# Performance work log

Measured on AMD Instinct MI355X. Metric: run time of the kernel, lower is better.

Reference implementation:

```python
import jax, jax.numpy as jnp
import numpy as np

N_USERS = 50000
N_ITEMS = 50000
N = N_USERS + N_ITEMS
C = 5        # n_criterion
D = 64       # emb_dim
A = 32       # att_dim
L = 2        # n_layers
E = 1600000  # edges per criterion
ALPHA = 0.3  # keras LeakyReLU default

def leaky(x):
    return jnp.where(x >= 0, x, ALPHA * x)

def setup_inputs() -> dict:
    key = jax.random.key(0)
    ks = jax.random.split(key, 11)
    return {
        "rows": jax.random.randint(ks[0], (C, E), 0, N),
        "cols": jax.random.randint(ks[1], (C, E), 0, N),
        "vals": jax.random.uniform(ks[2], (C, E), dtype=jnp.float32) * 0.01,
        "user_emb": 0.01 * jax.random.normal(ks[3], (N_USERS, C, D), dtype=jnp.float32),
        "item_emb": 0.01 * jax.random.normal(ks[4], (N_ITEMS, C, D), dtype=jnp.float32),
        "cri_emb": 0.01 * jax.random.normal(ks[5], (C, D), dtype=jnp.float32),
        "w_gcn": 0.01 * jax.random.normal(ks[6], (D, D), dtype=jnp.float32),
        "W_gc": 0.01 * jax.random.normal(ks[7], (L, D, D), dtype=jnp.float32),
        "W_rel": 0.01 * jax.random.normal(ks[8], (L, D, D), dtype=jnp.float32),
        "W1": 0.01 * jax.random.normal(ks[9], (C, D, A), dtype=jnp.float32),
        "W2": 0.01 * jax.random.normal(ks[10], (C, A), dtype=jnp.float32),
    }

def _spmm(r, c, v, x):
    # one criterion: sparse [N,N] (COO r,c,v) @ dense x [N,D]
    return jax.ops.segment_sum(v[:, None] * x[c], r, num_segments=N)

def reference(rows, cols, vals, user_emb, item_emb, cri_emb, w_gcn, W_gc, W_rel, W1, W2):
    pre = jnp.concatenate([user_emb, item_emb], axis=0)  # [N, C, D]
    acc = pre
    cri_cur = cri_emb                                    # [C, D]
    cri_hist = [cri_cur]
    for k in range(L):
        x = jnp.swapaxes(pre, 0, 1)                      # [C, N, D]
        emb = jax.vmap(_spmm)(rows, cols, vals, x)       # [C, N, D]
        emb = emb @ w_gcn                                # per-criterion dense transform
        emb = leaky((emb * cri_cur[:, None, :]) @ W_gc[k])
        emb_st = jnp.swapaxes(emb, 0, 1)                 # [N, C, D]
        # attention over criteria, one (W1,W2) pair per output criterion i
        s = jnp.einsum('ncd,ida->nica', emb_st, W1)      # [N, C_out, C_in, A]
        s = jnp.einsum('nica,ia->nic', jnp.tanh(s), W2)  # [N, C_out, C_in]
        attn = jax.nn.softmax(s, axis=2)
        pre = leaky(jnp.einsum('nic,ncd->nid', attn, emb_st))  # [N, C, D]
        acc = acc + pre                                  # dropout inactive (training=False)
        cri_cur = leaky(cri_cur @ W_rel[k])
        cri_hist.append(cri_cur)
    acc = acc / (L + 1)
    users = acc[:N_USERS]
    items = jnp.concatenate([acc[N_USERS:], jnp.zeros((1, C, D), acc.dtype)], axis=0)
    cri_mean = jnp.mean(jnp.stack(cri_hist, axis=0), axis=0)  # [C, D]
    return users, items, cri_mean
```

## Files before the change

kernel.cpp:

```cpp
#include <hip/hip_runtime.h>
#include <hip/hip_bf16.h>

#define NU      50000
#define NT      100000
#define NPADR   100032
#define NC      5
#define DD      64
#define AA      32
#define EE      1600000
#define CE      (NC*EE)
#define ROWF    (NC*DD)
#define NBL     1563
#define OUT_ELEMS 32000000

#define NBIN    782
#define BROWS   128
#define SBLK    250
#define EPB     6400
#define EPT     25
#define KTOT    (NC*NBIN*SBLK)
#define S1B     1910
#define LCAP    2560

#define TMP_OFF   0
#define XB_OFF    64020480
#define EBIN_OFF  128040960
#define HW_OFF    192040960
#define BSUM_OFF  195950960
#define BST_OFF   195958600
#define CRI1_OFF  195974244
#define WC_OFF    195975536
#define W1B_OFF   196057456

using short8 = __attribute__((ext_vector_type(8))) short;
using f32x4  = __attribute__((ext_vector_type(4))) float;

__device__ __forceinline__ f32x4 mfma16(short8 a, short8 b, f32x4 c){
  return __builtin_amdgcn_mfma_f32_16x16x32_bf16(a, b, c, 0, 0, 0);
}
__device__ __forceinline__ float lk(float x){ return x >= 0.f ? x : 0.3f*x; }
__device__ __forceinline__ float fast_tanh(float x){
  float e = __expf(2.0f*x);
  return (e - 1.0f) * __builtin_amdgcn_rcpf(e + 1.0f);
}
__device__ __forceinline__ float bf2f(unsigned u){ return __uint_as_float(u << 16); }
__device__ __forceinline__ unsigned short f2bf_rn(float f){
  unsigned b = __float_as_uint(f);
  return (unsigned short)((b + 0x7FFFu + ((b >> 16) & 1u)) >> 16);
}

__global__ __launch_bounds__(256) void dmcr_cvt(const float* __restrict__ ue,
                                                const float* __restrict__ ie,
                                                unsigned short* __restrict__ xb){
  size_t idx = ((size_t)blockIdx.x*256 + threadIdx.x) * 4;
  const float* src = (idx < (size_t)NU*ROWF) ? (ue + idx) : (ie + (idx - (size_t)NU*ROWF));
  float4 f = *(const float4*)src;
  ushort4 h;
  h.x = f2bf_rn(f.x); h.y = f2bf_rn(f.y); h.z = f2bf_rn(f.z); h.w = f2bf_rn(f.w);
  *(ushort4*)(xb + idx) = h;
}

__global__ __launch_bounds__(256) void dmcr_hist(const int* __restrict__ rows,
                                                 unsigned* __restrict__ hw){
  __shared__ unsigned hist[NBIN];
  const int c = blockIdx.y, blk = blockIdx.x, t = threadIdx.x;
  for (int i=t; i<NBIN; i+=256) hist[i] = 0u;
  __syncthreads();
  const size_t g0 = (size_t)c*EE + (size_t)blk*EPB;
  #pragma unroll
  for (int k=0; k<EPT; k++){
    int r = rows[g0 + t + k*256];
    atomicAdd(&hist[r>>7], 1u);
  }
  __syncthreads();
  unsigned* dst = hw + (size_t)(c*SBLK + blk)*NBIN;
  for (int i=t; i<NBIN; i+=256) dst[i] = hist[i];
}

__global__ __launch_bounds__(512) void dmcr_scan1(unsigned* __restrict__ hw,
                                                  unsigned* __restrict__ bsum){
  __shared__ unsigned sh[512];
  const int t = threadIdx.x; const int s = blockIdx.x*512 + t;
  unsigned v = 0u; size_t st = 0; const bool ok = (s < KTOT);
  if (ok){
    int c = s / (NBIN*SBLK); int rem = s - c*(NBIN*SBLK);
    int bin = rem / SBLK;    int blk = rem - bin*SBLK;
    st = (size_t)(c*SBLK + blk)*NBIN + bin;
    v = hw[st];
  }
  sh[t] = v; __syncthreads();
  for (int off=1; off<512; off<<=1){
    unsigned x = (t>=off) ? sh[t-off] : 0u; __syncthreads();
    sh[t] += x; __syncthreads();
  }
  if (ok) hw[st] = sh[t] - v;
  if (t == 511) bsum[blockIdx.x] = sh[511];
}
__global__ __launch_bounds__(1024) void dmcr_scan2(unsigned* __restrict__ bsum){
  __shared__ unsigned sh[1024];
  const int t = threadIdx.x;
  unsigned v0 = (2*t   < S1B) ? bsum[2*t]   : 0u;
  unsigned v1 = (2*t+1 < S1B) ? bsum[2*t+1] : 0u;
  unsigned p = v0 + v1;
  sh[t] = p; __syncthreads();
  for (int off=1; off<1024; off<<=1){
    unsigned x = (t>=off) ? sh[t-off] : 0u; __syncthreads();
    sh[t] += x; __syncthreads();
  }
  unsigned base = sh[t] - p;
  if (2*t   < S1B) bsum[2*t]   = base;
  if (2*t+1 < S1B) bsum[2*t+1] = base + v0;
}
__global__ __launch_bounds__(512) void dmcr_scan3(unsigned* __restrict__ hw,
                                                  const unsigned* __restrict__ bsum,
                                                  unsigned* __restrict__ bst){
  const int t = threadIdx.x; const int s = blockIdx.x*512 + t;
  if (s >= KTOT) return;
  int c = s / (NBIN*SBLK); int rem = s - c*(NBIN*SBLK);
  int bin = rem / SBLK;    int blk = rem - bin*SBLK;
  size_t st = (size_t)(c*SBLK + blk)*NBIN + bin;
  unsigned val = hw[st] + bsum[blockIdx.x];
  hw[st] = val;
  if (blk == 0) bst[c*NBIN + bin] = val;
  if (s == 0)   bst[NC*NBIN] = (unsigned)CE;
}

__global__ __launch_bounds__(256) void dmcr_sort(const int* __restrict__ rows,
                                                 const int* __restrict__ cols,
                                                 const float* __restrict__ vals,
                                                 const unsigned* __restrict__ hw,
                                                 uint2* __restrict__ eb2){
  __shared__ unsigned hist[1024];
  __shared__ unsigned sp[256];
  __shared__ unsigned gbl[NBIN];
  __shared__ uint2 staged[EPB];
  const int c = blockIdx.y, blk = blockIdx.x, t = threadIdx.x;
  for (int i=t; i<1024; i+=256) hist[i] = 0u;
  const size_t g0 = (size_t)c*EE + (size_t)blk*EPB;
  unsigned er[EPT], ep[EPT], rk[EPT];
  #pragma unroll
  for (int k=0; k<EPT; k++){
    size_t g = g0 + t + k*256;
    int r = rows[g];
    unsigned q = (unsigned)(vals[g]*819100.0f + 0.5f); q = q > 8191u ? 8191u : q;
    er[k] = (unsigned)r;
    ep[k] = (((unsigned)cols[g]) << 13) | q;
  }
  __syncthreads();
  #pragma unroll
  for (int k=0; k<EPT; k++) rk[k] = atomicAdd(&hist[er[k]>>7], 1u);
  __syncthreads();
  unsigned h[4]; unsigned psum = 0u;
  #pragma unroll
  for (int i=0; i<4; i++){ h[i] = hist[t*4+i]; psum += h[i]; }
  sp[t] = psum; __syncthreads();
  for (int off=1; off<256; off<<=1){
    unsigned x = (t>=off) ? sp[t-off] : 0u; __syncthreads();
    sp[t] += x; __syncthreads();
  }
  unsigned run = sp[t] - psum;
  #pragma unroll
  for (int i=0; i<4; i++){ hist[t*4+i] = run; run += h[i]; }
  const unsigned* gsrc = hw + (size_t)(c*SBLK + blk)*NBIN;
  for (int i=t; i<NBIN; i+=256) gbl[i] = gsrc[i];
  __syncthreads();
  #pragma unroll
  for (int k=0; k<EPT; k++){
    unsigned bin = er[k] >> 7;
    staged[hist[bin] + rk[k]] = make_uint2(ep[k], er[k]);
  }
  __syncthreads();
  #pragma unroll
  for (int k=0; k<EPT; k++){
    int pos = t + k*256;
    uint2 e = staged[pos];
    unsigned bin = e.y >> 7;
    unsigned dst = gbl[bin] + ((unsigned)pos - hist[bin]);
    eb2[dst] = e;
  }
}

__global__ __launch_bounds__(320) void dmcr_cri(const float* __restrict__ cri0,
                                                const float* __restrict__ Wrel,
                                                float* __restrict__ cri1_ws,
                                                float* __restrict__ outp){
  __shared__ float s0[320], s1[320];
  const int t = threadIdx.x; const int c = t>>6, d = t&63;
  float v0 = cri0[t];
  s0[t] = v0; __syncthreads();
  float a = 0.f;
  #pragma unroll
  for (int k=0;k<DD;k++) a += s0[c*DD+k] * Wrel[k*DD + d];
  float v1 = lk(a); s1[t] = v1; cri1_ws[t] = v1; __syncthreads();
  float b = 0.f;
  #pragma unroll
  for (int k=0;k<DD;k++) b += s1[c*DD+k] * Wrel[DD*DD + k*DD + d];
  float v2 = lk(b);
  outp[OUT_ELEMS + 320 + t] = (v0 + v1 + v2) * (1.f/3.f);
  outp[OUT_ELEMS + t] = 0.f;
}

__global__ __launch_bounds__(64) void dmcr_wc(const float* __restrict__ cri0,
                                              const float* __restrict__ cri1,
                                              const float* __restrict__ wgcn,
                                              const float* __restrict__ Wgc,
                                              unsigned short* __restrict__ WcB){
  __shared__ float wcl[64][65];
  const int b = blockIdx.x; const int l = b/5, c = b%5; const int j = threadIdx.x;
  const float* cri = (l==0 ? cri0 : cri1) + c*DD;
  float tt[DD];
  #pragma unroll
  for (int d=0; d<DD; d++) tt[d] = cri[d] * Wgc[l*DD*DD + d*DD + j];
  for (int i=0; i<DD; i++){
    float a = 0.f;
    #pragma unroll
    for (int d=0; d<DD; d++) a += wgcn[i*DD+d] * tt[d];
    wcl[i][j] = a;
  }
  __syncthreads();
  const int l15 = j&15, lg = j>>4;
  #pragma unroll
  for (int f=0; f<8; f++){
    const int nt = f>>1, kh = f&1;
    unsigned pk0, pk1, pk2, pk3;
    {
      unsigned short h0 = f2bf_rn(wcl[kh*32 + lg*8 + 0][nt*16 + l15]);
      unsigned short h1 = f2bf_rn(wcl[kh*32 + lg*8 + 1][nt*16 + l15]);
      pk0 = (unsigned)h0 | ((unsigned)h1 << 16);
      h0 = f2bf_rn(wcl[kh*32 + lg*8 + 2][nt*16 + l15]);
      h1 = f2bf_rn(wcl[kh*32 + lg*8 + 3][nt*16 + l15]);
      pk1 = (unsigned)h0 | ((unsigned)h1 << 16);
      h0 = f2bf_rn(wcl[kh*32 + lg*8 + 4][nt*16 + l15]);
      h1 = f2bf_rn(wcl[kh*32 + lg*8 + 5][nt*16 + l15]);
      pk2 = (unsigned)h0 | ((unsigned)h1 << 16);
      h0 = f2bf_rn(wcl[kh*32 + lg*8 + 6][nt*16 + l15]);
      h1 = f2bf_rn(wcl[kh*32 + lg*8 + 7][nt*16 + l15]);
      pk3 = (unsigned)h0 | ((unsigned)h1 << 16);
    }
    uint4 u; u.x=pk0; u.y=pk1; u.z=pk2; u.w=pk3;
    *(uint4*)(WcB + ((size_t)(b*8 + f)*64 + j)*8) = u;
  }
}

__global__ __launch_bounds__(64) void dmcr_w1b(const float* __restrict__ W1,
                                               unsigned short* __restrict__ W1B){
  __shared__ float wl[64][33];
  const int i = blockIdx.x; const int tdx = threadIdx.x;
  for (int r=0; r<32; r++){
    int e = r*64 + tdx;
    wl[e>>5][e&31] = W1[i*DD*AA + e];
  }
  __syncthreads();
  const int l15 = tdx&15, lg = tdx>>4;
  #pragma unroll
  for (int f=0; f<4; f++){
    const int nt = f>>1, kh = f&1;
    unsigned pk0, pk1, pk2, pk3;
    {
      unsigned short h0 = f2bf_rn(wl[kh*32 + lg*8 + 0][nt*16 + l15]);
      unsigned short h1 = f2bf_rn(wl[kh*32 + lg*8 + 1][nt*16 + l15]);
      pk0 = (unsigned)h0 | ((unsigned)h1 << 16);
      h0 = f2bf_rn(wl[kh*32 + lg*8 + 2][nt*16 + l15]);
      h1 = f2bf_rn(wl[kh*32 + lg*8 + 3][nt*16 + l15]);
      pk1 = (unsigned)h0 | ((unsigned)h1 << 16);
      h0 = f2bf_rn(wl[kh*32 + lg*8 + 4][nt*16 + l15]);
      h1 = f2bf_rn(wl[kh*32 + lg*8 + 5][nt*16 + l15]);
      pk2 = (unsigned)h0 | ((unsigned)h1 << 16);
      h0 = f2bf_rn(wl[kh*32 + lg*8 + 6][nt*16 + l15]);
      h1 = f2bf_rn(wl[kh*32 + lg*8 + 7][nt*16 + l15]);
      pk3 = (unsigned)h0 | ((unsigned)h1 << 16);
    }
    uint4 u; u.x=pk0; u.y=pk1; u.z=pk2; u.w=pk3;
    *(uint4*)(W1B + ((size_t)(i*4 + f)*64 + tdx)*8) = u;
  }
}

__global__ __launch_bounds__(256) void dmcr_spmm(const unsigned* __restrict__ bst,
                                                 const uint2* __restrict__ eb2,
                                                 const unsigned short* __restrict__ xb,
                                                 unsigned short* __restrict__ tmp16){
  __shared__ unsigned sorted[LCAP];
  __shared__ unsigned rh[BROWS];
  __shared__ unsigned ro[BROWS];
  const int c = blockIdx.y, b = blockIdx.x, t = threadIdx.x;
  const int idx = c*NBIN + b;
  const unsigned S = bst[idx];
  unsigned m = bst[idx+1] - S;
  m = m < (unsigned)LCAP ? m : (unsigned)LCAP;
  for (int i=t; i<BROWS; i+=256) rh[i] = 0u;
  __syncthreads();
  unsigned pay[10], rl[10], rk[10];
  #pragma unroll
  for (int k=0; k<10; k++){
    unsigned i = (unsigned)t + (unsigned)(k<<8);
    if (i < m){
      uint2 e = eb2[S + i];
      pay[k] = e.x; rl[k] = e.y & 127u;
      rk[k] = atomicAdd(&rh[rl[k]], 1u);
    }
  }
  __syncthreads();
  if (t < BROWS) ro[t] = rh[t];
  __syncthreads();
  for (int off=1; off<BROWS; off<<=1){
    unsigned x = 0u;
    if (t < BROWS && t >= off) x = ro[t-off];
    __syncthreads();
    if (t < BROWS) ro[t] += x;
    __syncthreads();
  }
  #pragma unroll
  for (int k=0; k<10; k++){
    unsigned i = (unsigned)t + (unsigned)(k<<8);
    if (i < m){
      unsigned r = rl[k];
      sorted[ro[r] - rh[r] + rk[k]] = pay[k];
    }
  }
  __syncthreads();
  const int w = t>>6, lane = t&63;
  const int co = c*DD + lane;
  for (int ri=0; ri<32; ri++){
    const int r = w*32 + ri;
    const unsigned cntr = rh[r];
    const unsigned beg = ro[r] - cntr;
    float acc = 0.f;
    unsigned j = 0;
    for (; j+2 <= cntr; j += 2){
      unsigned p0 = sorted[beg+j], p1 = sorted[beg+j+1];
      float v0 = (float)(p0 & 8191u) * (0.01f/8191.f);
      float v1 = (float)(p1 & 8191u) * (0.01f/8191.f);
      float x0 = bf2f(xb[(size_t)(p0 >> 13)*ROWF + co]);
      float x1 = bf2f(xb[(size_t)(p1 >> 13)*ROWF + co]);
      acc = fmaf(v0, x0, acc);
      acc = fmaf(v1, x1, acc);
    }
    if (j < cntr){
      unsigned p0 = sorted[beg+j];
      float v0 = (float)(p0 & 8191u) * (0.01f/8191.f);
      float x0 = bf2f(xb[(size_t)(p0 >> 13)*ROWF + co]);
      acc = fmaf(v0, x0, acc);
    }
    const int row = b*BROWS + r;
    if (row < NPADR) tmp16[(size_t)row*ROWF + co] = f2bf_rn(acc);
  }
}

#define SHS 328
__global__ __launch_bounds__(320, 4) void dmcr_layer(const unsigned short* __restrict__ tmp16,
                                                     const unsigned short* __restrict__ WcB,
                                                     const unsigned short* __restrict__ W1B,
                                                     const float* __restrict__ W2,
                                                     float* __restrict__ outp,
                                                     unsigned short* __restrict__ xb,
                                                     const float* __restrict__ ue,
                                                     const float* __restrict__ ie,
                                                     int layer){
  __shared__ unsigned short sh16[64*SHS];
  __shared__ float sx[1600];
  const int t = threadIdx.x;
  const int w = __builtin_amdgcn_readfirstlane(t >> 6);
  const int lane = t & 63;
  const int l15 = lane & 15, lg = lane >> 4;
  const size_t base = (size_t)blockIdx.x * (64*ROWF);

  short8 wcf[8];
  {
    const uint4* wp = (const uint4*)WcB + ((size_t)(layer*NC + w)*8)*64 + lane;
    #pragma unroll
    for (int f=0; f<8; f++){ uint4 u = wp[(size_t)f*64]; wcf[f] = *(short8*)&u; }
  }

  #pragma unroll
  for (int j = 0; j < 8; j++){
    int e = j*2560 + t*8;
    uint4 pk = *(const uint4*)(tmp16 + base + e);
    int n = e / ROWF, q = e % ROWF;
    *(uint4*)(sh16 + n*SHS + q) = pk;
  }
  __syncthreads();

  f32x4 c1[4][4];
  #pragma unroll
  for (int mt=0;mt<4;mt++)
    #pragma unroll
    for (int nt=0;nt<4;nt++) c1[mt][nt] = (f32x4){0.f,0.f,0.f,0.f};
  #pragma unroll
  for (int kh=0; kh<2; kh++)
    #pragma unroll
    for (int mt=0; mt<4; mt++){
      short8 a = *(const short8*)(sh16 + (mt*16+l15)*SHS + w*DD + kh*32 + lg*8);
      #pragma unroll
      for (int nt=0; nt<4; nt++) c1[mt][nt] = mfma16(a, wcf[nt*2+kh], c1[mt][nt]);
    }
  #pragma unroll
  for (int mt=0;mt<4;mt++)
    #pragma unroll
    for (int nt=0;nt<4;nt++)
      #pragma unroll
      for (int r=0;r<4;r++)
        sh16[(mt*16 + lg*4 + r)*SHS + w*DD + nt*16 + l15] = f2bf_rn(lk(c1[mt][nt][r]));

  short8 ea[2][4];
  #pragma unroll
  for (int kh=0;kh<2;kh++)
    #pragma unroll
    for (int mt=0;mt<4;mt++)
      ea[kh][mt] = *(const short8*)(sh16 + (mt*16+l15)*SHS + w*DD + kh*32 + lg*8);

  #pragma unroll 1
  for (int i=0;i<5;i++){
    short8 w1f[4];
    {
      const uint4* wp = (const uint4*)W1B + (size_t)(i*4)*64 + lane;
      #pragma unroll
      for (int f=0; f<4; f++){ uint4 u = wp[(size_t)f*64]; w1f[f] = *(short8*)&u; }
    }
    float w2a = W2[i*AA + l15];
    float w2b = W2[i*AA + 16 + l15];
    f32x4 c2[4][2];
    #pragma unroll
    for (int mt=0;mt<4;mt++){ c2[mt][0]=(f32x4){0.f,0.f,0.f,0.f}; c2[mt][1]=(f32x4){0.f,0.f,0.f,0.f}; }
    #pragma unroll
    for (int kh=0;kh<2;kh++)
      #pragma unroll
      for (int mt=0;mt<4;mt++){
        c2[mt][0] = mfma16(ea[kh][mt], w1f[0+kh], c2[mt][0]);
        c2[mt][1] = mfma16(ea[kh][mt], w1f[2+kh], c2[mt][1]);
      }
    #pragma unroll
    for (int mt=0;mt<4;mt++){
      float vr[4];
      #pragma unroll
      for (int r=0;r<4;r++){
        float v = fast_tanh(c2[mt][0][r])*w2a + fast_tanh(c2[mt][1][r])*w2b;
        v += __shfl_xor(v,1); v += __shfl_xor(v,2); v += __shfl_xor(v,4); v += __shfl_xor(v,8);
        vr[r] = v;
      }
      int rr = lane & 3;
      float vs = (rr==0) ? vr[0] : (rr==1) ? vr[1] : (rr==2) ? vr[2] : vr[3];
      if (l15 < 4) sx[i*320 + w*64 + mt*16 + lg*4 + rr] = vs;
    }
  }
  __syncthreads();

  float acc[64];
  {
    float sv[5];
    #pragma unroll
    for (int c = 0; c < 5; c++) sv[c] = sx[w*320 + c*64 + lane];
    float m = fmaxf(fmaxf(fmaxf(sv[0],sv[1]),fmaxf(sv[2],sv[3])),sv[4]);
    float at[5]; float ssum = 0.f;
    #pragma unroll
    for (int c = 0; c < 5; c++){ at[c] = __expf(sv[c]-m); ssum += at[c]; }
    float inv = __builtin_amdgcn_rcpf(ssum);
    #pragma unroll
    for (int d = 0; d < 64; d++) acc[d] = 0.f;
    #pragma unroll 1
    for (int c = 0; c < 5; c++){
      float a = at[c] * inv;
      const uint4* src = (const uint4*)(sh16 + lane*SHS + c*DD);
      #pragma unroll
      for (int g = 0; g < 8; g++){
        uint4 pk = src[g];
        acc[g*8+0] = fmaf(a, __uint_as_float(pk.x << 16),        acc[g*8+0]);
        acc[g*8+1] = fmaf(a, __uint_as_float(pk.x & 0xffff0000u), acc[g*8+1]);
        acc[g*8+2] = fmaf(a, __uint_as_float(pk.y << 16),        acc[g*8+2]);
        acc[g*8+3] = fmaf(a, __uint_as_float(pk.y & 0xffff0000u), acc[g*8+3]);
        acc[g*8+4] = fmaf(a, __uint_as_float(pk.z << 16),        acc[g*8+4]);
        acc[g*8+5] = fmaf(a, __uint_as_float(pk.z & 0xffff0000u), acc[g*8+5]);
        acc[g*8+6] = fmaf(a, __uint_as_float(pk.w << 16),        acc[g*8+6]);
        acc[g*8+7] = fmaf(a, __uint_as_float(pk.w & 0xffff0000u), acc[g*8+7]);
      }
    }
    #pragma unroll
    for (int d = 0; d < 64; d++) acc[d] = lk(acc[d]);
  }
  __syncthreads();
  {
    unsigned short* shr = sh16 + lane*SHS + w*DD;
    #pragma unroll
    for (int d = 0; d < 64; d++) shr[d] = f2bf_rn(acc[d]);
  }
  __syncthreads();

  #pragma unroll
  for (int j = 0; j < 8; j++){
    int e = j*2560 + t*8;
    size_t gidx = base + e;
    if (gidx >= (size_t)OUT_ELEMS) continue;
    int n = e / ROWF, q = e % ROWF;
    uint4 pk = *(const uint4*)(sh16 + n*SHS + q);
    float v[8];
    v[0]=__uint_as_float(pk.x<<16); v[1]=__uint_as_float(pk.x&0xffff0000u);
    v[2]=__uint_as_float(pk.y<<16); v[3]=__uint_as_float(pk.y&0xffff0000u);
    v[4]=__uint_as_float(pk.z<<16); v[5]=__uint_as_float(pk.z&0xffff0000u);
    v[6]=__uint_as_float(pk.w<<16); v[7]=__uint_as_float(pk.w&0xffff0000u);
    if (layer == 1){
      const float* p0 = (gidx < (size_t)NU*ROWF) ? (ue + gidx) : (ie + (gidx - (size_t)NU*ROWF));
      #pragma unroll
      for (int r = 0; r < 8; r += 4){
        float4 a0 = *(const float4*)(p0 + r);
        float4 o0 = *(const float4*)(outp + gidx + r);
        float4 ov;
        ov.x = (v[r+0] + a0.x + o0.x) * (1.f/3.f);
        ov.y = (v[r+1] + a0.y + o0.y) * (1.f/3.f);
        ov.z = (v[r+2] + a0.z + o0.z) * (1.f/3.f);
        ov.w = (v[r+3] + a0.w + o0.w) * (1.f/3.f);
        *(float4*)(outp + gidx + r) = ov;
      }
    } else {
      #pragma unroll
      for (int r = 0; r < 8; r += 4){
        float4 ov; ov.x = v[r+0]; ov.y = v[r+1]; ov.z = v[r+2]; ov.w = v[r+3];
        *(float4*)(outp + gidx + r) = ov;
      }
      *(uint4*)(xb + gidx) = pk;
    }
  }
}

extern "C" void kernel_launch(void* const* d_in, const int* in_sizes, int n_in,
                              void* d_out, int out_size, void* d_ws, size_t ws_size,
                              hipStream_t stream) {
  const int*   rows = (const int*)  d_in[0];
  const int*   cols = (const int*)  d_in[1];
  const float* vals = (const float*)d_in[2];
  const float* ue   = (const float*)d_in[3];
  const float* ie   = (const float*)d_in[4];
  const float* cri0 = (const float*)d_in[5];
  const float* wgcn = (const float*)d_in[6];
  const float* Wgc  = (const float*)d_in[7];
  const float* Wrel = (const float*)d_in[8];
  const float* W1   = (const float*)d_in[9];
  const float* W2   = (const float*)d_in[10];
  float* outp = (float*)d_out;
  char*  ws   = (char*)d_ws;

  unsigned short* tmp16 = (unsigned short*)(ws + TMP_OFF);
  unsigned short* xb    = (unsigned short*)(ws + XB_OFF);
  uint2*          eb2   = (uint2*)         (ws + EBIN_OFF);
  unsigned*       hw    = (unsigned*)      (ws + HW_OFF);
  unsigned*       bsum  = (unsigned*)      (ws + BSUM_OFF);
  unsigned*       bst   = (unsigned*)      (ws + BST_OFF);
  float*          cri1  = (float*)         (ws + CRI1_OFF);
  unsigned short* WcB   = (unsigned short*)(ws + WC_OFF);
  unsigned short* W1B   = (unsigned short*)(ws + W1B_OFF);

  dmcr_cvt  <<<31250, 256, 0, stream>>>(ue, ie, xb);
  dmcr_hist <<<dim3(SBLK, NC), 256, 0, stream>>>(rows, hw);
  dmcr_scan1<<<S1B, 512, 0, stream>>>(hw, bsum);
  dmcr_scan2<<<1, 1024, 0, stream>>>(bsum);
  dmcr_scan3<<<S1B, 512, 0, stream>>>(hw, bsum, bst);
  dmcr_sort <<<dim3(SBLK, NC), 256, 0, stream>>>(rows, cols, vals, hw, eb2);

  dmcr_cri<<<1, 320, 0, stream>>>(cri0, Wrel, cri1, outp);
  dmcr_wc <<<10, 64, 0, stream>>>(cri0, cri1, wgcn, Wgc, WcB);
  dmcr_w1b<<<5, 64, 0, stream>>>(W1, W1B);

  dmcr_spmm <<<dim3(NBIN, NC), 256, 0, stream>>>(bst, eb2, xb, tmp16);
  dmcr_layer<<<NBL, 320, 0, stream>>>(tmp16, WcB, W1B, W2, outp, xb, ue, ie, 0);

  dmcr_spmm <<<dim3(NBIN, NC), 256, 0, stream>>>(bst, eb2, xb, tmp16);
  dmcr_layer<<<NBL, 320, 0, stream>>>(tmp16, WcB, W1B, W2, outp, xb, ue, ie, 1);
}
```

Before: 1.218 ms.

## Precompute CSR row order once and simplify SpMM to streaming gathers

Adds a one-time sort pass that orders each bin's edges by local row and by a high-bit key from the payload (column bits), then writes a compact 4-byte payload array plus per-row start offsets. Both SpMM launches then skip the per-call shared-memory histogram, scan and scatter, loading presorted payloads directly and unrolling the gather loop by four. Sub-sorting by column within a row may improve locality of the xb gathers. The cost is an extra kernel and memory pass, and the 8-byte edge buffer now aliases the tmp16 region, which is safe only because it is consumed before the first SpMM writes tmp16.

```diff
diff --git a/kernel.cpp b/kernel.cpp
--- a/kernel.cpp
+++ b/kernel.cpp
@@ -15,6 +15,7 @@
 
 #define NBIN    782
 #define BROWS   128
+#define NROWP   (NBIN*BROWS)
 #define SBLK    250
 #define EPB     6400
 #define EPT     25
@@ -24,13 +25,14 @@
 
 #define TMP_OFF   0
 #define XB_OFF    64020480
-#define EBIN_OFF  128040960
-#define HW_OFF    192040960
-#define BSUM_OFF  195950960
-#define BST_OFF   195958600
-#define CRI1_OFF  195974244
-#define WC_OFF    195975536
-#define W1B_OFF   196057456
+#define EBP_OFF   128040960
+#define RS_OFF    160040960
+#define HW_OFF    162042884
+#define BSUM_OFF  165952884
+#define BST_OFF   165960524
+#define CRI1_OFF  165976168
+#define WC_OFF    165977456
+#define W1B_OFF   166059376
 
 using short8 = __attribute__((ext_vector_type(8))) short;
 using f32x4  = __attribute__((ext_vector_type(4))) float;
@@ -178,6 +180,55 @@
     unsigned dst = gbl[bin] + ((unsigned)pos - hist[bin]);
     eb2[dst] = e;
   }
+}
+
+__global__ __launch_bounds__(256) void dmcr_sort2(const unsigned* __restrict__ bst,
+                                                  const uint2* __restrict__ eb2,
+                                                  unsigned* __restrict__ ebp,
+                                                  unsigned* __restrict__ rs){
+  __shared__ unsigned h2[1024];
+  __shared__ unsigned sp[256];
+  __shared__ unsigned stg[LCAP];
+  const int c = blockIdx.y, b = blockIdx.x, t = threadIdx.x;
+  const int idx = c*NBIN + b;
+  const unsigned S = bst[idx];
+  unsigned m = bst[idx+1] - S;
+  m = m < (unsigned)LCAP ? m : (unsigned)LCAP;
+  for (int i=t; i<1024; i+=256) h2[i] = 0u;
+  __syncthreads();
+  unsigned pay[10], ky[10], rk[10];
+  #pragma unroll
+  for (int k=0; k<10; k++){
+    unsigned i = (unsigned)t + (unsigned)(k<<8);
+    if (i < m){
+      uint2 e = eb2[S + i];
+      pay[k] = e.x;
+      ky[k] = ((e.y & 127u) << 3) | (e.x >> 27);
+      rk[k] = atomicAdd(&h2[ky[k]], 1u);
+    }
+  }
+  __syncthreads();
+  unsigned h[4]; unsigned ps = 0u;
+  #pragma unroll
+  for (int i=0; i<4; i++){ h[i] = h2[t*4+i]; ps += h[i]; }
+  sp[t] = ps; __syncthreads();
+  for (int off=1; off<256; off<<=1){
+    unsigned x = (t>=off) ? sp[t-off] : 0u; __syncthreads();
+    sp[t] += x; __syncthreads();
+  }
+  unsigned run = sp[t] - ps;
+  #pragma unroll
+  for (int i=0; i<4; i++){ h2[t*4+i] = run; run += h[i]; }
+  __syncthreads();
+  if (t < BROWS) rs[(size_t)c*NROWP + (size_t)b*BROWS + t] = S + h2[t<<3];
+  if (c == NC-1 && b == NBIN-1 && t == 0) rs[(size_t)NC*NROWP] = (unsigned)CE;
+  #pragma unroll
+  for (int k=0; k<10; k++){
+    unsigned i = (unsigned)t + (unsigned)(k<<8);
+    if (i < m) stg[h2[ky[k]] + rk[k]] = pay[k];
+  }
+  __syncthreads();
+  for (unsigned i=t; i<m; i+=256) ebp[S + i] = stg[i];
 }
 
 __global__ __launch_bounds__(320) void dmcr_cri(const float* __restrict__ cri0,
@@ -276,70 +327,45 @@
 }
 
 __global__ __launch_bounds__(256) void dmcr_spmm(const unsigned* __restrict__ bst,
-                                                 const uint2* __restrict__ eb2,
+                                                 const unsigned* __restrict__ rs,
+                                                 const unsigned* __restrict__ ebp,
                                                  const unsigned short* __restrict__ xb,
                                                  unsigned short* __restrict__ tmp16){
-  __shared__ unsigned sorted[LCAP];
-  __shared__ unsigned rh[BROWS];
-  __shared__ unsigned ro[BROWS];
+  __shared__ unsigned pl[LCAP];
+  __shared__ unsigned rsl[BROWS+1];
   const int c = blockIdx.y, b = blockIdx.x, t = threadIdx.x;
   const int idx = c*NBIN + b;
   const unsigned S = bst[idx];
   unsigned m = bst[idx+1] - S;
   m = m < (unsigned)LCAP ? m : (unsigned)LCAP;
-  for (int i=t; i<BROWS; i+=256) rh[i] = 0u;
-  __syncthreads();
-  unsigned pay[10], rl[10], rk[10];
-  #pragma unroll
-  for (int k=0; k<10; k++){
-    unsigned i = (unsigned)t + (unsigned)(k<<8);
-    if (i < m){
-      uint2 e = eb2[S + i];
-      pay[k] = e.x; rl[k] = e.y & 127u;
-      rk[k] = atomicAdd(&rh[rl[k]], 1u);
-    }
-  }
-  __syncthreads();
-  if (t < BROWS) ro[t] = rh[t];
-  __syncthreads();
-  for (int off=1; off<BROWS; off<<=1){
-    unsigned x = 0u;
-    if (t < BROWS && t >= off) x = ro[t-off];
-    __syncthreads();
-    if (t < BROWS) ro[t] += x;
-    __syncthreads();
-  }
-  #pragma unroll
-  for (int k=0; k<10; k++){
-    unsigned i = (unsigned)t + (unsigned)(k<<8);
-    if (i < m){
-      unsigned r = rl[k];
-      sorted[ro[r] - rh[r] + rk[k]] = pay[k];
-    }
+  for (unsigned i=t; i<m; i+=256) pl[i] = ebp[S+i];
+  if (t <= BROWS){
+    unsigned v = rs[(size_t)c*NROWP + (size_t)b*BROWS + t] - S;
+    rsl[t] = v < m ? v : m;
   }
   __syncthreads();
   const int w = t>>6, lane = t&63;
   const int co = c*DD + lane;
   for (int ri=0; ri<32; ri++){
-    const int r = w*32 + ri;
-    const unsigned cntr = rh[r];
-    const unsigned beg = ro[r] - cntr;
+    const int r = (w<<5) + ri;
+    const unsigned beg = rsl[r], end = rsl[r+1];
     float acc = 0.f;
-    unsigned j = 0;
-    for (; j+2 <= cntr; j += 2){
-      unsigned p0 = sorted[beg+j], p1 = sorted[beg+j+1];
-      float v0 = (float)(p0 & 8191u) * (0.01f/8191.f);
-      float v1 = (float)(p1 & 8191u) * (0.01f/8191.f);
+    unsigned j = beg;
+    for (; j+4 <= end; j += 4){
+      unsigned p0=pl[j], p1=pl[j+1], p2=pl[j+2], p3=pl[j+3];
       float x0 = bf2f(xb[(size_t)(p0 >> 13)*ROWF + co]);
       float x1 = bf2f(xb[(size_t)(p1 >> 13)*ROWF + co]);
-      acc = fmaf(v0, x0, acc);
-      acc = fmaf(v1, x1, acc);
-    }
-    if (j < cntr){
-      unsigned p0 = sorted[beg+j];
-      float v0 = (float)(p0 & 8191u) * (0.01f/8191.f);
+      float x2 = bf2f(xb[(size_t)(p2 >> 13)*ROWF + co]);
+      float x3 = bf2f(xb[(size_t)(p3 >> 13)*ROWF + co]);
+      acc = fmaf((float)(p0 & 8191u)*(0.01f/8191.f), x0, acc);
+      acc = fmaf((float)(p1 & 8191u)*(0.01f/8191.f), x1, acc);
+      acc = fmaf((float)(p2 & 8191u)*(0.01f/8191.f), x2, acc);
+      acc = fmaf((float)(p3 & 8191u)*(0.01f/8191.f), x3, acc);
+    }
+    for (; j < end; j++){
+      unsigned p0 = pl[j];
       float x0 = bf2f(xb[(size_t)(p0 >> 13)*ROWF + co]);
-      acc = fmaf(v0, x0, acc);
+      acc = fmaf((float)(p0 & 8191u)*(0.01f/8191.f), x0, acc);
     }
     const int row = b*BROWS + r;
     if (row < NPADR) tmp16[(size_t)row*ROWF + co] = f2bf_rn(acc);
@@ -538,8 +564,10 @@
   char*  ws   = (char*)d_ws;
 
   unsigned short* tmp16 = (unsigned short*)(ws + TMP_OFF);
+  uint2*          eb2   = (uint2*)         (ws + TMP_OFF);
   unsigned short* xb    = (unsigned short*)(ws + XB_OFF);
-  uint2*          eb2   = (uint2*)         (ws + EBIN_OFF);
+  unsigned*       ebp   = (unsigned*)      (ws + EBP_OFF);
+  unsigned*       rs    = (unsigned*)      (ws + RS_OFF);
   unsigned*       hw    = (unsigned*)      (ws + HW_OFF);
   unsigned*       bsum  = (unsigned*)      (ws + BSUM_OFF);
   unsigned*       bst   = (unsigned*)      (ws + BST_OFF);
@@ -553,14 +581,15 @@
   dmcr_scan2<<<1, 1024, 0, stream>>>(bsum);
   dmcr_scan3<<<S1B, 512, 0, stream>>>(hw, bsum, bst);
   dmcr_sort <<<dim3(SBLK, NC), 256, 0, stream>>>(rows, cols, vals, hw, eb2);
+  dmcr_sort2<<<dim3(NBIN, NC), 256, 0, stream>>>(bst, eb2, ebp, rs);
 
   dmcr_cri<<<1, 320, 0, stream>>>(cri0, Wrel, cri1, outp);
   dmcr_wc <<<10, 64, 0, stream>>>(cri0, cri1, wgcn, Wgc, WcB);
   dmcr_w1b<<<5, 64, 0, stream>>>(W1, W1B);
 
-  dmcr_spmm <<<dim3(NBIN, NC), 256, 0, stream>>>(bst, eb2, xb, tmp16);
+  dmcr_spmm <<<dim3(NBIN, NC), 256, 0, stream>>>(bst, rs, ebp, xb, tmp16);
   dmcr_layer<<<NBL, 320, 0, stream>>>(tmp16, WcB, W1B, W2, outp, xb, ue, ie, 0);
 
-  dmcr_spmm <<<dim3(NBIN, NC), 256, 0, stream>>>(bst, eb2, xb, tmp16);
+  dmcr_spmm <<<dim3(NBIN, NC), 256, 0, stream>>>(bst, rs, ebp, xb, tmp16);
   dmcr_layer<<<NBL, 320, 0, stream>>>(tmp16, WcB, W1B, W2, outp, xb, ue, ie, 1);
 }
```

Result: faster. 1.103 ms (-9.4%).
